# Performance work log

Measured on AMD Instinct MI355X. Metric: run time of the kernel, lower is better.

## Reference

```python
import jax, jax.numpy as jnp
import numpy as np

N = 50000
E = 800000
H = 2          # heads
C = 64         # out channels per head (embedding_size)
NEG_SLOPE = 0.2


def setup_inputs() -> dict:
    key = jax.random.key(0)
    ks = jax.random.split(key, 8)
    x = jax.random.normal(ks[0], (N, 1), dtype=jnp.float32)
    edge_index = jax.random.randint(ks[1], (2, E), 0, N, dtype=jnp.int64)
    edge_attr = jax.random.normal(ks[2], (E, 1), dtype=jnp.float32)
    # GATv2Conv params: lin_l, lin_r (with bias), lin_edge (no bias), att, out bias
    W_l = jax.random.normal(ks[3], (1, H * C), dtype=jnp.float32)
    b_l = jnp.zeros((H * C,), dtype=jnp.float32)
    W_r = jax.random.normal(ks[4], (1, H * C), dtype=jnp.float32)
    b_r = jnp.zeros((H * C,), dtype=jnp.float32)
    W_e = jax.random.normal(ks[5], (1, H * C), dtype=jnp.float32)
    att = jax.random.normal(ks[6], (H, C), dtype=jnp.float32)
    bias = jnp.zeros((H * C,), dtype=jnp.float32)
    return {"x": x, "edge_index": edge_index, "edge_attr": edge_attr,
            "W_l": W_l, "b_l": b_l, "W_r": W_r, "b_r": b_r,
            "W_e": W_e, "att": att, "bias": bias}


def reference(x, edge_index, edge_attr, W_l, b_l, W_r, b_r, W_e, att, bias):
    n = x.shape[0]
    src, dst = edge_index[0], edge_index[1]

    # add_self_loops=True with fill_value='mean': self-loop edge_attr at node i
    # is the mean of incoming edge_attr (0 if no incoming edges).
    attr_sum = jax.ops.segment_sum(edge_attr, dst, num_segments=n)      # [N,1]
    cnt = jax.ops.segment_sum(jnp.ones((src.shape[0], 1), edge_attr.dtype), dst, num_segments=n)
    loop_attr = attr_sum / jnp.maximum(cnt, 1.0)                         # [N,1]

    loop = jnp.arange(n, dtype=src.dtype)
    src_f = jnp.concatenate([src, loop])                                 # [E+N]
    dst_f = jnp.concatenate([dst, loop])
    attr_f = jnp.concatenate([edge_attr, loop_attr], axis=0)             # [E+N,1]

    x_l = (x @ W_l + b_l).reshape(n, H, C)    # source transform
    x_r = (x @ W_r + b_r).reshape(n, H, C)    # target transform
    e = (attr_f @ W_e).reshape(-1, H, C)      # edge feature embedding

    # GATv2 attention: leaky_relu(x_l[j] + x_r[i] + e) . att
    g = jax.nn.leaky_relu(x_l[src_f] + x_r[dst_f] + e, NEG_SLOPE)        # [E+N,H,C]
    logits = jnp.einsum('ehc,hc->eh', g, att)                            # [E+N,H]

    # segment softmax grouped by destination node
    mx = jax.ops.segment_max(logits, dst_f, num_segments=n)              # [N,H]
    a = jnp.exp(logits - mx[dst_f])
    den = jax.ops.segment_sum(a, dst_f, num_segments=n)                  # [N,H]
    alpha = a / den[dst_f]                                               # [E+N,H]

    # weighted scatter-add of source messages
    out = jax.ops.segment_sum(alpha[:, :, None] * x_l[src_f], dst_f, num_segments=n)  # [N,H,C]
    return out.reshape(n, H * C) + bias
```

## Files before the change

### kernel.cpp

```cpp
#include <hip/hip_runtime.h>

#define NEG 0.2f

__device__ __forceinline__ float leaky(float v){ return fmaxf(v, NEG * v); }

__global__ void __launch_bounds__(256) k_edge(
        const int* __restrict__ src, const int* __restrict__ dst,
        const float* __restrict__ attr, const float* __restrict__ x,
        const float* __restrict__ Wl, const float* __restrict__ Wr,
        const float* __restrict__ We, const float* __restrict__ bl,
        const float* __restrict__ br, const float* __restrict__ att,
        int* __restrict__ head, int* __restrict__ nxt,
        float4* __restrict__ payload, int E){
    const int sub = threadIdx.x & 15;
    const float4* Wl4 = (const float4*)Wl;
    const float4* Wr4 = (const float4*)Wr;
    const float4* We4 = (const float4*)We;
    const float4* bl4 = (const float4*)bl;
    const float4* br4 = (const float4*)br;
    const float4* at4 = (const float4*)att;
    const int q = sub * 2;
    float4 wl0 = Wl4[q], wl1 = Wl4[q+1];
    float4 wr0 = Wr4[q], wr1 = Wr4[q+1];
    float4 we0 = We4[q], we1 = We4[q+1];
    float4 b0  = bl4[q], b1  = bl4[q+1];
    float4 c0  = br4[q], c1  = br4[q+1];
    float4 a0  = at4[q], a1  = at4[q+1];
    b0.x += c0.x; b0.y += c0.y; b0.z += c0.z; b0.w += c0.w;
    b1.x += c1.x; b1.y += c1.y; b1.z += c1.z; b1.w += c1.w;

    const int gid     = (blockIdx.x * 256 + threadIdx.x) >> 4;
    const int ngroups = (gridDim.x * 256) >> 4;

    for (int e = gid; e < E; e += ngroups){
        int s = src[e], d = dst[e];
        float xs = x[s], xd = x[d], a = attr[e];
        float acc;
        {
            float v0 = fmaf(xs, wl0.x, fmaf(xd, wr0.x, fmaf(a, we0.x, b0.x)));
            float v1 = fmaf(xs, wl0.y, fmaf(xd, wr0.y, fmaf(a, we0.y, b0.y)));
            float v2 = fmaf(xs, wl0.z, fmaf(xd, wr0.z, fmaf(a, we0.z, b0.z)));
            float v3 = fmaf(xs, wl0.w, fmaf(xd, wr0.w, fmaf(a, we0.w, b0.w)));
            acc  = leaky(v0) * a0.x;
            acc  = fmaf(leaky(v1), a0.y, acc);
            acc  = fmaf(leaky(v2), a0.z, acc);
            acc  = fmaf(leaky(v3), a0.w, acc);
            v0 = fmaf(xs, wl1.x, fmaf(xd, wr1.x, fmaf(a, we1.x, b1.x)));
            v1 = fmaf(xs, wl1.y, fmaf(xd, wr1.y, fmaf(a, we1.y, b1.y)));
            v2 = fmaf(xs, wl1.z, fmaf(xd, wr1.z, fmaf(a, we1.z, b1.z)));
            v3 = fmaf(xs, wl1.w, fmaf(xd, wr1.w, fmaf(a, we1.w, b1.w)));
            acc  = fmaf(leaky(v0), a1.x, acc);
            acc  = fmaf(leaky(v1), a1.y, acc);
            acc  = fmaf(leaky(v2), a1.z, acc);
            acc  = fmaf(leaky(v3), a1.w, acc);
        }
        acc += __shfl_xor(acc, 1);
        acc += __shfl_xor(acc, 2);
        acc += __shfl_xor(acc, 4);
        float other = __shfl_xor(acc, 8);
        if (sub == 0){
            payload[e] = make_float4(xs, a, acc, other);
            int prev = atomicExch(&head[d], e);
            nxt[e] = prev;
        }
    }
}

__global__ void __launch_bounds__(256) k_walk(
        const float* __restrict__ x,
        const int* __restrict__ head, const int* __restrict__ nxt,
        const float4* __restrict__ payload,
        const float* __restrict__ Wl, const float* __restrict__ Wr,
        const float* __restrict__ We, const float* __restrict__ bl,
        const float* __restrict__ br, const float* __restrict__ att,
        float* __restrict__ sres, int N){
    __shared__ float4 pk[128];
    int t = threadIdx.x;
    if (t < 128)
        pk[t] = make_float4(Wl[t] + Wr[t], We[t], bl[t] + br[t], att[t]);
    __syncthreads();

    int i = blockIdx.x * 256 + t;
    if (i >= N) return;
    float m0 = -3.4e38f, d0 = 0.f, n0 = 0.f;
    float m1 = -3.4e38f, d1 = 0.f, n1 = 0.f;
    float asum = 0.f;
    int deg = 0;
    for (int e = head[i]; e >= 0; e = nxt[e]){
        float4 v = payload[e];
        ++deg;
        asum += v.y;
        float mn0 = fmaxf(m0, v.z);
        float s0 = __expf(m0 - mn0), p0 = __expf(v.z - mn0);
        d0 = fmaf(d0, s0, p0);
        n0 = fmaf(n0, s0, p0 * v.x);
        m0 = mn0;
        float mn1 = fmaxf(m1, v.w);
        float s1 = __expf(m1 - mn1), p1 = __expf(v.w - mn1);
        d1 = fmaf(d1, s1, p1);
        n1 = fmaf(n1, s1, p1 * v.x);
        m1 = mn1;
    }
    float xi = x[i];
    float la = asum / (float)max(deg, 1);
    float l0 = 0.f, l1 = 0.f;
    #pragma unroll 8
    for (int c = 0; c < 64; ++c){
        float4 p = pk[c];
        float v = fmaf(xi, p.x, fmaf(la, p.y, p.z));
        l0 = fmaf(leaky(v), p.w, l0);
    }
    #pragma unroll 8
    for (int c = 64; c < 128; ++c){
        float4 p = pk[c];
        float v = fmaf(xi, p.x, fmaf(la, p.y, p.z));
        l1 = fmaf(leaky(v), p.w, l1);
    }
    {
        float mn = fmaxf(m0, l0);
        float s = __expf(m0 - mn), p = __expf(l0 - mn);
        d0 = fmaf(d0, s, p);
        n0 = fmaf(n0, s, p * xi);
    }
    {
        float mn = fmaxf(m1, l1);
        float s = __expf(m1 - mn), p = __expf(l1 - mn);
        d1 = fmaf(d1, s, p);
        n1 = fmaf(n1, s, p * xi);
    }
    sres[2 * i]     = n0 / d0;
    sres[2 * i + 1] = n1 / d1;
}

__global__ void __launch_bounds__(256) k_final4(
        const float* __restrict__ sres,
        const float* __restrict__ Wl, const float* __restrict__ bl,
        const float* __restrict__ bias,
        float4* __restrict__ out, int total4){
    int t = blockIdx.x * 256 + threadIdx.x;
    if (t >= total4) return;
    int i = t >> 5;
    int q = t & 31;
    int h = q >> 4;
    float s = sres[2 * i + h];
    float4 wv = ((const float4*)Wl)[q];
    float4 bv = ((const float4*)bl)[q];
    float4 zv = ((const float4*)bias)[q];
    out[t] = make_float4(fmaf(s, wv.x, bv.x + zv.x), fmaf(s, wv.y, bv.y + zv.y),
                         fmaf(s, wv.z, bv.z + zv.z), fmaf(s, wv.w, bv.w + zv.w));
}

extern "C" void kernel_launch(void* const* d_in, const int* in_sizes, int n_in,
                              void* d_out, int out_size, void* d_ws, size_t ws_size,
                              hipStream_t stream) {
    const float* x    = (const float*)d_in[0];
    const int*   ei   = (const int*)  d_in[1];
    const float* attr = (const float*)d_in[2];
    const float* Wl   = (const float*)d_in[3];
    const float* bl   = (const float*)d_in[4];
    const float* Wr   = (const float*)d_in[5];
    const float* br   = (const float*)d_in[6];
    const float* We   = (const float*)d_in[7];
    const float* att  = (const float*)d_in[8];
    const float* bias = (const float*)d_in[9];
    float* out = (float*)d_out;

    const int N = in_sizes[0];
    const int E = in_sizes[2];
    const int* src = ei;
    const int* dst = ei + E;

    char* w = (char*)d_ws;
    float4* payload = (float4*)w;
    int*    nxt     = (int*)(w + (size_t)E * 16);
    int*    head    = nxt + E;
    float*  sres    = (float*)(head + N);

    hipMemsetAsync(head, 0xFF, (size_t)N * sizeof(int), stream);

    k_edge<<<2048, 256, 0, stream>>>(src, dst, attr, x,
                                     Wl, Wr, We, bl, br, att,
                                     head, nxt, payload, E);
    k_walk<<<(N + 255) / 256, 256, 0, stream>>>(x, head, nxt, payload,
                                                Wl, Wr, We, bl, br, att,
                                                sres, N);
    k_final4<<<((size_t)N * 32 + 255) / 256, 256, 0, stream>>>(sres, Wl, bl, bias,
                                                               (float4*)out, N * 32);
}
```

Before: 89.87 us.

## Split per-node edge lists into four chains walked by four lanes

Each destination node now has four linked-list heads, chosen by edge index mod 4. The walk kernel assigns four lanes per node that traverse the chains in parallel and merge their online-softmax state with shuffles. The self-loop logit computation is also split across the four lanes. In the edge kernel the atomicExch is issued early and the payload/next stores become nontemporal. This is meant to shorten the serial pointer-chasing latency per node, at the cost of a larger head array to memset, more shuffle work and four times as many threads.

Result: faster. 86.22 us (-4.1%).

```diff
diff --git a/kernel.cpp b/kernel.cpp
--- a/kernel.cpp
+++ b/kernel.cpp
@@ -1,6 +1,8 @@
 #include <hip/hip_runtime.h>
 
 #define NEG 0.2f
+
+typedef float f4v __attribute__((ext_vector_type(4)));
 
 __device__ __forceinline__ float leaky(float v){ return fmaxf(v, NEG * v); }
 
@@ -10,7 +12,7 @@
         const float* __restrict__ Wl, const float* __restrict__ Wr,
         const float* __restrict__ We, const float* __restrict__ bl,
         const float* __restrict__ br, const float* __restrict__ att,
-        int* __restrict__ head, int* __restrict__ nxt,
+        int* __restrict__ head4, int* __restrict__ nxt,
         float4* __restrict__ payload, int E){
     const int sub = threadIdx.x & 15;
     const float4* Wl4 = (const float4*)Wl;
@@ -34,6 +36,9 @@
 
     for (int e = gid; e < E; e += ngroups){
         int s = src[e], d = dst[e];
+        int prev = 0;
+        if (sub == 0)
+            prev = atomicExch(&head4[(d << 2) + (e & 3)], e);
         float xs = x[s], xd = x[d], a = attr[e];
         float acc;
         {
@@ -59,16 +64,16 @@
         acc += __shfl_xor(acc, 4);
         float other = __shfl_xor(acc, 8);
         if (sub == 0){
-            payload[e] = make_float4(xs, a, acc, other);
-            int prev = atomicExch(&head[d], e);
-            nxt[e] = prev;
+            f4v pv = { xs, a, acc, other };
+            __builtin_nontemporal_store(pv, (f4v*)&payload[e]);
+            __builtin_nontemporal_store(prev, &nxt[e]);
         }
     }
 }
 
 __global__ void __launch_bounds__(256) k_walk(
         const float* __restrict__ x,
-        const int* __restrict__ head, const int* __restrict__ nxt,
+        const int* __restrict__ head4, const int* __restrict__ nxt,
         const float4* __restrict__ payload,
         const float* __restrict__ Wl, const float* __restrict__ Wr,
         const float* __restrict__ We, const float* __restrict__ bl,
@@ -80,13 +85,15 @@
         pk[t] = make_float4(Wl[t] + Wr[t], We[t], bl[t] + br[t], att[t]);
     __syncthreads();
 
-    int i = blockIdx.x * 256 + t;
+    int g = blockIdx.x * 256 + t;
+    int i = g >> 2, sub = g & 3;
     if (i >= N) return;
+
     float m0 = -3.4e38f, d0 = 0.f, n0 = 0.f;
     float m1 = -3.4e38f, d1 = 0.f, n1 = 0.f;
     float asum = 0.f;
     int deg = 0;
-    for (int e = head[i]; e >= 0; e = nxt[e]){
+    for (int e = head4[(i << 2) + sub]; e >= 0; e = nxt[e]){
         float4 v = payload[e];
         ++deg;
         asum += v.y;
@@ -101,35 +108,47 @@
         n1 = fmaf(n1, s1, p1 * v.x);
         m1 = mn1;
     }
+    #pragma unroll
+    for (int off = 1; off < 4; off <<= 1){
+        float om0 = __shfl_xor(m0, off), od0 = __shfl_xor(d0, off), on0 = __shfl_xor(n0, off);
+        float om1 = __shfl_xor(m1, off), od1 = __shfl_xor(d1, off), on1 = __shfl_xor(n1, off);
+        asum += __shfl_xor(asum, off);
+        deg  += __shfl_xor(deg, off);
+        float mn = fmaxf(m0, om0);
+        d0 = d0 * __expf(m0 - mn) + od0 * __expf(om0 - mn);
+        n0 = n0 * __expf(m0 - mn) + on0 * __expf(om0 - mn);
+        m0 = mn;
+        mn = fmaxf(m1, om1);
+        d1 = d1 * __expf(m1 - mn) + od1 * __expf(om1 - mn);
+        n1 = n1 * __expf(m1 - mn) + on1 * __expf(om1 - mn);
+        m1 = mn;
+    }
     float xi = x[i];
     float la = asum / (float)max(deg, 1);
-    float l0 = 0.f, l1 = 0.f;
+    float pl = 0.f;
     #pragma unroll 8
-    for (int c = 0; c < 64; ++c){
-        float4 p = pk[c];
+    for (int k = 0; k < 32; ++k){
+        float4 p = pk[sub * 32 + k];
         float v = fmaf(xi, p.x, fmaf(la, p.y, p.z));
-        l0 = fmaf(leaky(v), p.w, l0);
-    }
-    #pragma unroll 8
-    for (int c = 64; c < 128; ++c){
-        float4 p = pk[c];
-        float v = fmaf(xi, p.x, fmaf(la, p.y, p.z));
-        l1 = fmaf(leaky(v), p.w, l1);
-    }
-    {
+        pl = fmaf(leaky(v), p.w, pl);
+    }
+    pl += __shfl_xor(pl, 1);
+    int lane = threadIdx.x & 63;
+    int base = lane & ~3;
+    float l0 = __shfl(pl, base);
+    float l1 = __shfl(pl, base + 2);
+    if (sub == 0){
         float mn = fmaxf(m0, l0);
         float s = __expf(m0 - mn), p = __expf(l0 - mn);
         d0 = fmaf(d0, s, p);
         n0 = fmaf(n0, s, p * xi);
-    }
-    {
-        float mn = fmaxf(m1, l1);
-        float s = __expf(m1 - mn), p = __expf(l1 - mn);
+        mn = fmaxf(m1, l1);
+        s = __expf(m1 - mn); p = __expf(l1 - mn);
         d1 = fmaf(d1, s, p);
         n1 = fmaf(n1, s, p * xi);
-    }
-    sres[2 * i]     = n0 / d0;
-    sres[2 * i + 1] = n1 / d1;
+        sres[2 * i]     = n0 / d0;
+        sres[2 * i + 1] = n1 / d1;
+    }
 }
 
 __global__ void __launch_bounds__(256) k_final4(
@@ -173,17 +192,17 @@
     char* w = (char*)d_ws;
     float4* payload = (float4*)w;
     int*    nxt     = (int*)(w + (size_t)E * 16);
-    int*    head    = nxt + E;
-    float*  sres    = (float*)(head + N);
-
-    hipMemsetAsync(head, 0xFF, (size_t)N * sizeof(int), stream);
+    int*    head4   = nxt + E;
+    float*  sres    = (float*)(head4 + 4 * (size_t)N);
+
+    hipMemsetAsync(head4, 0xFF, (size_t)4 * N * sizeof(int), stream);
 
     k_edge<<<2048, 256, 0, stream>>>(src, dst, attr, x,
                                      Wl, Wr, We, bl, br, att,
-                                     head, nxt, payload, E);
-    k_walk<<<(N + 255) / 256, 256, 0, stream>>>(x, head, nxt, payload,
-                                                Wl, Wr, We, bl, br, att,
-                                                sres, N);
+                                     head4, nxt, payload, E);
+    k_walk<<<(4 * N + 255) / 256, 256, 0, stream>>>(x, head4, nxt, payload,
+                                                    Wl, Wr, We, bl, br, att,
+                                                    sres, N);
     k_final4<<<((size_t)N * 32 + 255) / 256, 256, 0, stream>>>(sres, Wl, bl, bias,
                                                                (float4*)out, N * 32);
 }
```
